# Kernel optimization log

Measured on AMD Instinct MI355X. Metric: run time of the kernel, lower is better.

The kernel has to match this reference:

```python
import jax, jax.numpy as jnp
import numpy as np

WINDOW_SIZE = 5
CONSISTENCY_WEIGHT = 1.0


def _wsum(x, w):
    # sliding-window sum along axis 1 via exclusive cumsum differences
    s = jnp.cumsum(x, axis=1)
    s = jnp.pad(s, ((0, 0), (1, 0)))
    return s[:, w:] - s[:, :-w]  # [B, L-w+1]


def setup_inputs() -> dict:
    key = jax.random.key(0)
    k1, k2, k3 = jax.random.split(key, 3)
    B, L, C = 512, 16384, 2
    return {
        "predictions": jax.random.normal(k1, (B, L, C), dtype=jnp.float32),
        "targets": jax.random.randint(k2, (B, L), 0, 2, dtype=jnp.int32),
        "mask": jax.random.randint(k3, (B, L), 0, 2, dtype=jnp.int32),
    }


def reference(predictions, targets, mask):
    w = WINDOW_SIZE
    probs = jax.nn.softmax(predictions, axis=-1)[..., 1]  # [B, L]
    t = targets.astype(jnp.float32)
    m = mask.astype(jnp.float32)

    msum = _wsum(m, w)                       # [B, W]
    denom = jnp.maximum(msum, 1.0)           # clamp(min=1.0)
    spm = _wsum(probs * m, w)
    stm = _wsum(t * m, w)
    sp2m = _wsum(probs * probs * m, w)
    st2m = _wsum(t * t * m, w)

    pmean = spm / denom
    tmean = stm / denom
    # masked biased variance: sum((x - mean)^2 * m) / clamp(msum, 1)
    pvar = (sp2m - 2.0 * pmean * spm + pmean * pmean * msum) / denom
    tvar = (st2m - 2.0 * tmean * stm + tmean * tmean * msum) / denom

    mse = jnp.mean((pvar - tvar) ** 2, axis=0)          # per-window MSE over batch, [W]
    valid = (jnp.sum(msum, axis=0) > 0).astype(jnp.float32)  # skip windows with zero mask
    cnt = jnp.maximum(jnp.sum(valid), 1.0)
    loss = jnp.sum(mse * valid) / cnt * CONSISTENCY_WEIGHT
    return loss
```

## Files before the change

### kernel.cpp

```cpp
#include <hip/hip_runtime.h>
#include <math.h>

#define BATCH 512
#define LEN   16384
#define WIN   5
#define WOUT  (LEN - WIN + 1)
#define TPB   256
#define WPT   4
#define WPB   (TPB * WPT)
#define EPT   (WPT + WIN - 1)
#define NCH2  16

__device__ __forceinline__ float fast_rcp(float x) {
    float r = __builtin_amdgcn_rcpf(x);
    return r * fmaf(-x, r, 2.0f);
}

__global__ __launch_bounds__(TPB, 8)
void bcl_partial_kernel(const float* __restrict__ pred,
                        const int*   __restrict__ tgt,
                        const int*   __restrict__ msk,
                        float* __restrict__ part_d2,
                        float* __restrict__ part_ms,
                        int bper) {
    const int j0 = blockIdx.x * WPB + (int)threadIdx.x * WPT;
    if (j0 >= WOUT) return;
    const int b0 = blockIdx.y * bper;

    float accd2[WPT] = {0.f, 0.f, 0.f, 0.f};
    float accms[WPT] = {0.f, 0.f, 0.f, 0.f};

    for (int b = b0; b < b0 + bper; ++b) {
        const size_t base = (size_t)b * LEN + j0;

        const int4 m0 = *(const int4*)(msk + base);
        const int4 m1 = *(const int4*)(msk + base + 4);
        const int4 t0 = *(const int4*)(tgt + base);
        const int4 t1 = *(const int4*)(tgt + base + 4);
        const float4 q0 = *(const float4*)(pred + base * 2);
        const float4 q1 = *(const float4*)(pred + base * 2 + 4);
        const float4 q2 = *(const float4*)(pred + base * 2 + 8);
        const float4 q3 = *(const float4*)(pred + base * 2 + 12);

        float m[EPT], tm[EPT], pm[EPT], p2m[EPT];
        {
            const int mi[EPT] = {m0.x, m0.y, m0.z, m0.w, m1.x, m1.y, m1.z, m1.w};
            const int ti[EPT] = {t0.x, t0.y, t0.z, t0.w, t1.x, t1.y, t1.z, t1.w};
            const float dx[EPT] = {q0.x - q0.y, q0.z - q0.w,
                                   q1.x - q1.y, q1.z - q1.w,
                                   q2.x - q2.y, q2.z - q2.w,
                                   q3.x - q3.y, q3.z - q3.w};
#pragma unroll
            for (int i = 0; i < EPT; ++i) {
                const float p  = fast_rcp(1.0f + __expf(dx[i]));
                const float mf = (float)mi[i];
                m[i]   = mf;
                tm[i]  = (float)(ti[i] & mi[i]);
                pm[i]  = p * mf;
                p2m[i] = p * p * mf;
            }
        }

#pragma unroll
        for (int w = 0; w < WPT; ++w) {
            float msum = 0.f, stm = 0.f, spm = 0.f, sp2m = 0.f;
#pragma unroll
            for (int k = 0; k < WIN; ++k) {
                msum += m[w + k];
                stm  += tm[w + k];
                spm  += pm[w + k];
                sp2m += p2m[w + k];
            }
            const float denom = fmaxf(msum, 1.0f);
            const float inv   = fast_rcp(denom);
            const float pmean = spm * inv;
            const float tmean = stm * inv;
            const float pvar  = (sp2m - 2.0f * pmean * spm + pmean * pmean * msum) * inv;
            const float tvar  = (stm  - 2.0f * tmean * stm + tmean * tmean * msum) * inv;
            const float d = pvar - tvar;
            accd2[w] += d * d;
            accms[w] += msum;
        }
    }

    *(float4*)(part_d2 + (size_t)blockIdx.y * WOUT + j0) =
        make_float4(accd2[0], accd2[1], accd2[2], accd2[3]);
    *(float4*)(part_ms + (size_t)blockIdx.y * WOUT + j0) =
        make_float4(accms[0], accms[1], accms[2], accms[3]);
}

__global__ __launch_bounds__(TPB)
void bcl_chunk_reduce(const float* __restrict__ part_d2,
                      const float* __restrict__ part_ms,
                      float* __restrict__ p2_d2,
                      float* __restrict__ p2_ms,
                      int rf) {
    const int j = blockIdx.x * blockDim.x + threadIdx.x;
    if (j >= WOUT) return;
    const int c0 = blockIdx.y * rf;
    float d2 = 0.f, ms = 0.f;
#pragma unroll 8
    for (int c = c0; c < c0 + rf; ++c) {
        d2 += part_d2[(size_t)c * WOUT + j];
        ms += part_ms[(size_t)c * WOUT + j];
    }
    p2_d2[(size_t)blockIdx.y * WOUT + j] = d2;
    p2_ms[(size_t)blockIdx.y * WOUT + j] = ms;
}

__global__ __launch_bounds__(TPB)
void bcl_window_reduce(const float* __restrict__ p2_d2,
                       const float* __restrict__ p2_ms,
                       double* __restrict__ accum,
                       unsigned int* __restrict__ ticket,
                       float* __restrict__ out,
                       int nch2) {
    const int j = blockIdx.x * blockDim.x + threadIdx.x;
    double num = 0.0, cnt = 0.0;
    if (j < WOUT) {
        float d2 = 0.f, ms = 0.f;
#pragma unroll 8
        for (int c = 0; c < nch2; ++c) {
            d2 += p2_d2[(size_t)c * WOUT + j];
            ms += p2_ms[(size_t)c * WOUT + j];
        }
        if (ms > 0.f) {
            num = (double)d2 * (1.0 / (double)BATCH);
            cnt = 1.0;
        }
    }
    for (int off = 32; off > 0; off >>= 1) {
        num += __shfl_down(num, off, 64);
        cnt += __shfl_down(cnt, off, 64);
    }
    __shared__ double s_num[4], s_cnt[4];
    const int lane = threadIdx.x & 63, wave = threadIdx.x >> 6;
    if (lane == 0) { s_num[wave] = num; s_cnt[wave] = cnt; }
    __syncthreads();
    if (threadIdx.x == 0) {
        double n = 0.0, c = 0.0;
        const int nw = (int)(blockDim.x >> 6);
        for (int wv = 0; wv < nw; ++wv) { n += s_num[wv]; c += s_cnt[wv]; }
        atomicAdd(&accum[0], n);
        atomicAdd(&accum[1], c);
        __threadfence();
        const unsigned int t = atomicAdd(ticket, 1u);
        if (t == gridDim.x - 1) {
            out[0] = (float)(accum[0] / fmax(accum[1], 1.0));
        }
    }
}

extern "C" void kernel_launch(void* const* d_in, const int* in_sizes, int n_in,
                              void* d_out, int out_size, void* d_ws, size_t ws_size,
                              hipStream_t stream) {
    const float* pred = (const float*)d_in[0];
    const int*   tgt  = (const int*)d_in[1];
    const int*   msk  = (const int*)d_in[2];
    float* out = (float*)d_out;

    int nchunks = 128;
    while (nchunks > 1) {
        size_t need = (size_t)(nchunks + NCH2) * WOUT * 2 * sizeof(float) + 256;
        if (need <= ws_size) break;
        nchunks >>= 1;
    }
    const int bper = BATCH / nchunks;
    const int nch2 = (nchunks >= NCH2) ? NCH2 : nchunks;
    const int rf   = nchunks / nch2;

    float* part_d2 = (float*)d_ws;
    float* part_ms = part_d2 + (size_t)nchunks * WOUT;
    float* p2_d2   = part_ms + (size_t)nchunks * WOUT;
    float* p2_ms   = p2_d2   + (size_t)NCH2 * WOUT;
    size_t off = ((size_t)((char*)(p2_ms + (size_t)NCH2 * WOUT) - (char*)d_ws) + 15) & ~(size_t)15;
    double* accum = (double*)((char*)d_ws + off);
    unsigned int* ticket = (unsigned int*)(accum + 2);

    hipMemsetAsync((void*)accum, 0, 2 * sizeof(double) + sizeof(unsigned int), stream);

    const int WBLKS = (WOUT + WPB - 1) / WPB;
    dim3 g1(WBLKS, nchunks);
    bcl_partial_kernel<<<g1, TPB, 0, stream>>>(pred, tgt, msk, part_d2, part_ms, bper);

    const int RBLKS = (WOUT + TPB - 1) / TPB;
    dim3 gA(RBLKS, nch2);
    bcl_chunk_reduce<<<gA, TPB, 0, stream>>>(part_d2, part_ms, p2_d2, p2_ms, rf);

    bcl_window_reduce<<<RBLKS, TPB, 0, stream>>>(p2_d2, p2_ms, accum, ticket, out, nch2);
}
```

Before: 166.0 us.

## Double-buffer row loads, halve chunk counts, fold memset into reduce kernel

The partial kernel now software-pipelines batch rows: it loads the next row's mask, target and prediction vectors while computing on the current one, and relaxes launch bounds to 4 waves per EU so the extra registers fit. Chunk counts drop (64 batch chunks, 8 second-level chunks), which shrinks the partial-sum traffic and the reduce work at the cost of fewer blocks in the first kernel. The separate memset launch is removed; the chunk-reduce kernel zeroes the accumulator and ticket instead, which is safe because window_reduce runs after it on the same stream. The pipelined loop assumes bper is even and at least 2.

```diff
diff --git a/kernel.cpp b/kernel.cpp
--- a/kernel.cpp
+++ b/kernel.cpp
@@ -9,14 +9,79 @@
 #define WPT   4
 #define WPB   (TPB * WPT)
 #define EPT   (WPT + WIN - 1)
-#define NCH2  16
+#define NCH2  8
 
 __device__ __forceinline__ float fast_rcp(float x) {
     float r = __builtin_amdgcn_rcpf(x);
     return r * fmaf(-x, r, 2.0f);
 }
 
-__global__ __launch_bounds__(TPB, 8)
+struct Row {
+    int4   m0, m1, t0, t1;
+    float4 q0, q1, q2, q3;
+};
+
+__device__ __forceinline__ Row load_row(const float* __restrict__ pred,
+                                        const int*   __restrict__ tgt,
+                                        const int*   __restrict__ msk,
+                                        size_t base) {
+    Row r;
+    r.m0 = *(const int4*)(msk + base);
+    r.m1 = *(const int4*)(msk + base + 4);
+    r.t0 = *(const int4*)(tgt + base);
+    r.t1 = *(const int4*)(tgt + base + 4);
+    r.q0 = *(const float4*)(pred + base * 2);
+    r.q1 = *(const float4*)(pred + base * 2 + 4);
+    r.q2 = *(const float4*)(pred + base * 2 + 8);
+    r.q3 = *(const float4*)(pred + base * 2 + 12);
+    return r;
+}
+
+__device__ __forceinline__ void accum_row(const Row& r,
+                                          float accd2[WPT], float accms[WPT]) {
+    float m[EPT], tm[EPT], pm[EPT], p2m[EPT];
+    {
+        const int mi[EPT] = {r.m0.x, r.m0.y, r.m0.z, r.m0.w,
+                             r.m1.x, r.m1.y, r.m1.z, r.m1.w};
+        const int ti[EPT] = {r.t0.x, r.t0.y, r.t0.z, r.t0.w,
+                             r.t1.x, r.t1.y, r.t1.z, r.t1.w};
+        const float dx[EPT] = {r.q0.x - r.q0.y, r.q0.z - r.q0.w,
+                               r.q1.x - r.q1.y, r.q1.z - r.q1.w,
+                               r.q2.x - r.q2.y, r.q2.z - r.q2.w,
+                               r.q3.x - r.q3.y, r.q3.z - r.q3.w};
+#pragma unroll
+        for (int i = 0; i < EPT; ++i) {
+            const float p  = fast_rcp(1.0f + __expf(dx[i]));
+            const float mf = (float)mi[i];
+            m[i]   = mf;
+            tm[i]  = (float)(ti[i] & mi[i]);
+            pm[i]  = p * mf;
+            p2m[i] = p * p * mf;
+        }
+    }
+#pragma unroll
+    for (int w = 0; w < WPT; ++w) {
+        float msum = 0.f, stm = 0.f, spm = 0.f, sp2m = 0.f;
+#pragma unroll
+        for (int k = 0; k < WIN; ++k) {
+            msum += m[w + k];
+            stm  += tm[w + k];
+            spm  += pm[w + k];
+            sp2m += p2m[w + k];
+        }
+        const float denom = fmaxf(msum, 1.0f);
+        const float inv   = fast_rcp(denom);
+        const float pmean = spm * inv;
+        const float tmean = stm * inv;
+        const float pvar  = (sp2m - 2.0f * pmean * spm + pmean * pmean * msum) * inv;
+        const float tvar  = (stm  - 2.0f * tmean * stm + tmean * tmean * msum) * inv;
+        const float d = pvar - tvar;
+        accd2[w] += d * d;
+        accms[w] += msum;
+    }
+}
+
+__global__ __launch_bounds__(TPB, 4)
 void bcl_partial_kernel(const float* __restrict__ pred,
                         const int*   __restrict__ tgt,
                         const int*   __restrict__ msk,
@@ -30,57 +95,21 @@
     float accd2[WPT] = {0.f, 0.f, 0.f, 0.f};
     float accms[WPT] = {0.f, 0.f, 0.f, 0.f};
 
-    for (int b = b0; b < b0 + bper; ++b) {
-        const size_t base = (size_t)b * LEN + j0;
-
-        const int4 m0 = *(const int4*)(msk + base);
-        const int4 m1 = *(const int4*)(msk + base + 4);
-        const int4 t0 = *(const int4*)(tgt + base);
-        const int4 t1 = *(const int4*)(tgt + base + 4);
-        const float4 q0 = *(const float4*)(pred + base * 2);
-        const float4 q1 = *(const float4*)(pred + base * 2 + 4);
-        const float4 q2 = *(const float4*)(pred + base * 2 + 8);
-        const float4 q3 = *(const float4*)(pred + base * 2 + 12);
-
-        float m[EPT], tm[EPT], pm[EPT], p2m[EPT];
-        {
-            const int mi[EPT] = {m0.x, m0.y, m0.z, m0.w, m1.x, m1.y, m1.z, m1.w};
-            const int ti[EPT] = {t0.x, t0.y, t0.z, t0.w, t1.x, t1.y, t1.z, t1.w};
-            const float dx[EPT] = {q0.x - q0.y, q0.z - q0.w,
-                                   q1.x - q1.y, q1.z - q1.w,
-                                   q2.x - q2.y, q2.z - q2.w,
-                                   q3.x - q3.y, q3.z - q3.w};
-#pragma unroll
-            for (int i = 0; i < EPT; ++i) {
-                const float p  = fast_rcp(1.0f + __expf(dx[i]));
-                const float mf = (float)mi[i];
-                m[i]   = mf;
-                tm[i]  = (float)(ti[i] & mi[i]);
-                pm[i]  = p * mf;
-                p2m[i] = p * p * mf;
-            }
-        }
-
-#pragma unroll
-        for (int w = 0; w < WPT; ++w) {
-            float msum = 0.f, stm = 0.f, spm = 0.f, sp2m = 0.f;
-#pragma unroll
-            for (int k = 0; k < WIN; ++k) {
-                msum += m[w + k];
-                stm  += tm[w + k];
-                spm  += pm[w + k];
-                sp2m += p2m[w + k];
-            }
-            const float denom = fmaxf(msum, 1.0f);
-            const float inv   = fast_rcp(denom);
-            const float pmean = spm * inv;
-            const float tmean = stm * inv;
-            const float pvar  = (sp2m - 2.0f * pmean * spm + pmean * pmean * msum) * inv;
-            const float tvar  = (stm  - 2.0f * tmean * stm + tmean * tmean * msum) * inv;
-            const float d = pvar - tvar;
-            accd2[w] += d * d;
-            accms[w] += msum;
-        }
+    size_t base = (size_t)b0 * LEN + j0;
+
+    Row A = load_row(pred, tgt, msk, base);
+
+    for (int it = 0; it + 2 < bper; it += 2) {
+        Row B = load_row(pred, tgt, msk, base + LEN);
+        accum_row(A, accd2, accms);
+        A = load_row(pred, tgt, msk, base + 2 * (size_t)LEN);
+        accum_row(B, accd2, accms);
+        base += 2 * (size_t)LEN;
+    }
+    {
+        Row B = load_row(pred, tgt, msk, base + LEN);
+        accum_row(A, accd2, accms);
+        accum_row(B, accd2, accms);
     }
 
     *(float4*)(part_d2 + (size_t)blockIdx.y * WOUT + j0) =
@@ -94,7 +123,12 @@
                       const float* __restrict__ part_ms,
                       float* __restrict__ p2_d2,
                       float* __restrict__ p2_ms,
+                      double* __restrict__ accum,
+                      unsigned int* __restrict__ ticket,
                       int rf) {
+    if (blockIdx.x == 0 && blockIdx.y == 0 && threadIdx.x == 0) {
+        accum[0] = 0.0; accum[1] = 0.0; *ticket = 0u;
+    }
     const int j = blockIdx.x * blockDim.x + threadIdx.x;
     if (j >= WOUT) return;
     const int c0 = blockIdx.y * rf;
@@ -159,8 +193,8 @@
     const int*   msk  = (const int*)d_in[2];
     float* out = (float*)d_out;
 
-    int nchunks = 128;
-    while (nchunks > 1) {
+    int nchunks = 64;
+    while (nchunks > 2) {
         size_t need = (size_t)(nchunks + NCH2) * WOUT * 2 * sizeof(float) + 256;
         if (need <= ws_size) break;
         nchunks >>= 1;
@@ -177,15 +211,14 @@
     double* accum = (double*)((char*)d_ws + off);
     unsigned int* ticket = (unsigned int*)(accum + 2);
 
-    hipMemsetAsync((void*)accum, 0, 2 * sizeof(double) + sizeof(unsigned int), stream);
-
     const int WBLKS = (WOUT + WPB - 1) / WPB;
     dim3 g1(WBLKS, nchunks);
     bcl_partial_kernel<<<g1, TPB, 0, stream>>>(pred, tgt, msk, part_d2, part_ms, bper);
 
     const int RBLKS = (WOUT + TPB - 1) / TPB;
     dim3 gA(RBLKS, nch2);
-    bcl_chunk_reduce<<<gA, TPB, 0, stream>>>(part_d2, part_ms, p2_d2, p2_ms, rf);
+    bcl_chunk_reduce<<<gA, TPB, 0, stream>>>(part_d2, part_ms, p2_d2, p2_ms,
+                                             accum, ticket, rf);
 
     bcl_window_reduce<<<RBLKS, TPB, 0, stream>>>(p2_d2, p2_ms, accum, ticket, out, nch2);
 }
```

New measurement: 174.9 us. 1.05x slower.
